# Kernel optimization log

Hardware: AMD Instinct MI355X
Metric: run time of the kernel (lower is better)

Reference implementation:

```python
import jax, jax.numpy as jnp
from jax import lax
import numpy as np

DIM = 8
C = 192
N = 198  # 2 special tokens + 14*14 patches (distilled=True)
B = 1024


def quick_gelu(x):
    return x * jax.nn.sigmoid(1.702 * x)


def setup_inputs() -> dict:
    key = jax.random.key(0)
    ks = jax.random.split(key, 7)
    return {
        "x": jax.random.normal(ks[0], (B, N, C), dtype=jnp.float32),
        "w_down": jax.random.normal(ks[1], (DIM, C), dtype=jnp.float32) * 0.05,
        "b_down": jnp.zeros((DIM,), dtype=jnp.float32),
        "conv_w": jax.random.normal(ks[2], (DIM, DIM, 3, 3), dtype=jnp.float32) * 0.05,
        "conv_b": jnp.zeros((DIM,), dtype=jnp.float32),
        "w_up": jax.random.normal(ks[3], (C, DIM), dtype=jnp.float32) * 0.05,
        "b_up": jnp.zeros((C,), dtype=jnp.float32),
    }


def _conv3x3(t, conv_w, conv_b):
    # t: [B, dim, H, W]; 3x3, stride 1, pad 1 (SAME)
    y = lax.conv_general_dilated(
        t, conv_w, window_strides=(1, 1), padding=((1, 1), (1, 1)),
        dimension_numbers=("NCHW", "OIHW", "NCHW"))
    return y + conv_b[None, :, None, None]


def reference(x, w_down, b_down, conv_w, conv_b, w_up, b_up):
    b, n, c = x.shape
    dim = w_down.shape[0]
    # down projection + QuickGELU
    d = quick_gelu(jnp.einsum("bnc,dc->bnd", x, w_down) + b_down)
    # patch tokens -> [B, dim, 14, 14] -> conv -> [B, 196, dim]
    x_patch = d[:, 2:].reshape(b, 14, 14, dim).transpose(0, 3, 1, 2)
    x_patch = _conv3x3(x_patch, conv_w, conv_b)
    x_patch = x_patch.transpose(0, 2, 3, 1).reshape(b, 14 * 14, dim)
    # cls token -> [B, dim, 1, 1] -> conv (only center tap contributes) -> [B, 1, dim]
    x_cls = d[:, :1].reshape(b, 1, 1, dim).transpose(0, 3, 1, 2)
    x_cls = _conv3x3(x_cls, conv_w, conv_b)
    x_cls = x_cls.transpose(0, 2, 3, 1).reshape(b, 1, dim)
    zero_dist = jnp.zeros_like(x_cls)
    d2 = jnp.concatenate([x_cls, zero_dist, x_patch], axis=1)
    d2 = quick_gelu(d2)  # dropout is identity in eval mode
    return jnp.einsum("bnd,cd->bnc", d2, w_up) + b_up
```

## Files before the change

### kernel.cpp

```cpp
#include <hip/hip_runtime.h>
#include <math.h>

#define NTOK 198
#define CCH  192

typedef float vf4 __attribute__((ext_vector_type(4)));

__device__ __forceinline__ float qgelu(float v) {
    return v / (1.0f + __expf(-1.702f * v));
}

__device__ __forceinline__ float dot8(const float4& a, const float4& wa,
                                      const float4& b, const float4& wb) {
    return a.x*wa.x + a.y*wa.y + a.z*wa.z + a.w*wa.w
         + b.x*wb.x + b.y*wb.y + b.z*wb.z + b.w*wb.w;
}

__global__ __launch_bounds__(512, 4) void convpass_fused(
    const float* __restrict__ x,
    const float* __restrict__ w_down,
    const float* __restrict__ b_down,
    const float* __restrict__ conv_w,
    const float* __restrict__ conv_b,
    const float* __restrict__ w_up,
    const float* __restrict__ b_up,
    float* __restrict__ out)
{
    const int b   = blockIdx.x;
    const int tid = threadIdx.x;

    __shared__ float s_d[NTOK * 8];
    __shared__ float s_d2[NTOK * 8];
    __shared__ float s_cw[576];
    __shared__ float s_cb[8];

    for (int t = tid; t < 576; t += 512) {
        const int kk = t >> 6, rem = t & 63, o = rem >> 3, i = rem & 7;
        s_cw[t] = conv_w[(o * 8 + i) * 9 + kk];
    }
    if (tid < 8) s_cb[tid] = conv_b[tid];

    {
        const int lane  = tid & 63;
        const int wv    = tid >> 6;
        const int chunk = lane >> 3;
        const int dim   = lane & 7;

        float wreg[24];
        {
            const float* wp = w_down + dim * CCH + chunk * 24;
            #pragma unroll
            for (int j = 0; j < 24; ++j) wreg[j] = wp[j];
        }
        const float bd  = b_down[dim];
        const float* xb = x + (size_t)b * NTOK * CCH + chunk * 24;

        const int nIter = (NTOK - wv + 7) >> 3;
        #pragma unroll 1
        for (int i = 0; i < nIter; ++i) {
            const int idx = i * 8 + wv;
            const bool valid = (idx < NTOK);
            const int n = valid ? idx : 0;
            const float* xr = xb + (size_t)n * CCH;
            float a0 = 0.f, a1 = 0.f;
            #pragma unroll
            for (int j = 0; j < 3; ++j) {
                const float4 xv = *(const float4*)(xr + j * 8);
                const float4 xw = *(const float4*)(xr + j * 8 + 4);
                a0 += xv.x*wreg[j*8]   + xv.y*wreg[j*8+1] + xv.z*wreg[j*8+2] + xv.w*wreg[j*8+3];
                a1 += xw.x*wreg[j*8+4] + xw.y*wreg[j*8+5] + xw.z*wreg[j*8+6] + xw.w*wreg[j*8+7];
            }
            float acc = a0 + a1;
            acc += __shfl_xor(acc, 8);
            acc += __shfl_xor(acc, 16);
            acc += __shfl_xor(acc, 32);
            if (valid && lane < 8) s_d[idx * 8 + dim] = qgelu(acc + bd);
        }
    }
    __syncthreads();

    for (int j = tid; j < NTOK * 4; j += 512) {
        const int n = j >> 2, o2 = j & 3;
        const int oA = o2, oB = o2 + 4;
        if (n == 1) {
            s_d2[n * 8 + oA] = 0.0f;
            s_d2[n * 8 + oB] = 0.0f;
        } else if (n == 0) {
            const float4 d0 = *(const float4*)&s_d[0];
            const float4 d1 = *(const float4*)&s_d[4];
            const float4 wa0 = *(const float4*)&s_cw[4 * 64 + oA * 8];
            const float4 wa1 = *(const float4*)&s_cw[4 * 64 + oA * 8 + 4];
            const float4 wb0 = *(const float4*)&s_cw[4 * 64 + oB * 8];
            const float4 wb1 = *(const float4*)&s_cw[4 * 64 + oB * 8 + 4];
            s_d2[n * 8 + oA] = qgelu(s_cb[oA] + dot8(d0, wa0, d1, wa1));
            s_d2[n * 8 + oB] = qgelu(s_cb[oB] + dot8(d0, wb0, d1, wb1));
        } else {
            const int pos = n - 2, h = pos / 14, w = pos % 14;
            float accA = s_cb[oA];
            float accB = s_cb[oB];
            #pragma unroll
            for (int dh = -1; dh <= 1; ++dh) {
                const int hh = h + dh;
                if (hh < 0 || hh > 13) continue;
                #pragma unroll
                for (int dw = -1; dw <= 1; ++dw) {
                    const int ww = w + dw;
                    if (ww < 0 || ww > 13) continue;
                    const int tok = 2 + hh * 14 + ww;
                    const int kk  = (dh + 1) * 3 + (dw + 1);
                    const float4 d0 = *(const float4*)&s_d[tok * 8];
                    const float4 d1 = *(const float4*)&s_d[tok * 8 + 4];
                    const float4 wa0 = *(const float4*)&s_cw[kk * 64 + oA * 8];
                    const float4 wa1 = *(const float4*)&s_cw[kk * 64 + oA * 8 + 4];
                    const float4 wb0 = *(const float4*)&s_cw[kk * 64 + oB * 8];
                    const float4 wb1 = *(const float4*)&s_cw[kk * 64 + oB * 8 + 4];
                    accA += dot8(d0, wa0, d1, wa1);
                    accB += dot8(d0, wb0, d1, wb1);
                }
            }
            s_d2[n * 8 + oA] = qgelu(accA);
            s_d2[n * 8 + oB] = qgelu(accB);
        }
    }
    __syncthreads();

    const int c4 = tid % 48;
    const int tl = tid / 48;
    if (tl < 10) {
        float w_r[4][8];
        #pragma unroll
        for (int cc = 0; cc < 4; ++cc) {
            const float4 wa = *(const float4*)(w_up + (c4 * 4 + cc) * 8);
            const float4 wb = *(const float4*)(w_up + (c4 * 4 + cc) * 8 + 4);
            w_r[cc][0] = wa.x; w_r[cc][1] = wa.y; w_r[cc][2] = wa.z; w_r[cc][3] = wa.w;
            w_r[cc][4] = wb.x; w_r[cc][5] = wb.y; w_r[cc][6] = wb.z; w_r[cc][7] = wb.w;
        }
        const float4 bu = *(const float4*)(b_up + c4 * 4);
        float* outb = out + (size_t)b * NTOK * CCH;
        #pragma unroll 1
        for (int nr = tl; nr < NTOK; nr += 10) {
            const float4 da = *(const float4*)&s_d2[nr * 8];
            const float4 dv = *(const float4*)&s_d2[nr * 8 + 4];
            float accs[4] = {bu.x, bu.y, bu.z, bu.w};
            #pragma unroll
            for (int cc = 0; cc < 4; ++cc) {
                accs[cc] += da.x * w_r[cc][0] + da.y * w_r[cc][1]
                          + da.z * w_r[cc][2] + da.w * w_r[cc][3]
                          + dv.x * w_r[cc][4] + dv.y * w_r[cc][5]
                          + dv.z * w_r[cc][6] + dv.w * w_r[cc][7];
            }
            const vf4 r = {accs[0], accs[1], accs[2], accs[3]};
            __builtin_nontemporal_store(r, (vf4*)(outb + (size_t)nr * CCH + c4 * 4));
        }
    }
}

extern "C" void kernel_launch(void* const* d_in, const int* in_sizes, int n_in,
                              void* d_out, int out_size, void* d_ws, size_t ws_size,
                              hipStream_t stream) {
    const float* x      = (const float*)d_in[0];
    const float* w_down = (const float*)d_in[1];
    const float* b_down = (const float*)d_in[2];
    const float* conv_w = (const float*)d_in[3];
    const float* conv_b = (const float*)d_in[4];
    const float* w_up   = (const float*)d_in[5];
    const float* b_up   = (const float*)d_in[6];
    float* out = (float*)d_out;

    const int B = in_sizes[0] / (NTOK * CCH);
    convpass_fused<<<dim3(B), dim3(512), 0, stream>>>(
        x, w_down, b_down, conv_w, conv_b, w_up, b_up, out);
}
```

Before: 75.73 us.

## Split each batch across two blocks along tokens with halo recomputation

Launches two blocks per batch element, each handling about half of the output tokens. Each block recomputes the down-projection for the extra rows of tokens the 3x3 conv needs at the split boundary, and shared-memory buffers shrink to match. The aim is more and smaller blocks, giving better load balance and more overlap between the down-projection, conv and up-projection phases across the GPU. The cost is redundant reads of about 26 rows of x per batch and extra down-projection compute.

Result: slower. 83.68 us (+10.5%).

```diff
diff --git a/kernel.cpp b/kernel.cpp
--- a/kernel.cpp
+++ b/kernel.cpp
@@ -26,11 +26,17 @@
     const float* __restrict__ b_up,
     float* __restrict__ out)
 {
-    const int b   = blockIdx.x;
-    const int tid = threadIdx.x;
+    const int half = blockIdx.x & 1;
+    const int b    = blockIdx.x >> 1;
+    const int tid  = threadIdx.x;
 
-    __shared__ float s_d[NTOK * 8];
-    __shared__ float s_d2[NTOK * 8];
+    const int d_start   = half ? 86  : 0;
+    const int d_count   = half ? 112 : 114;
+    const int out_start = half ? 100 : 0;
+    const int out_count = half ? 98  : 100;
+
+    __shared__ float s_d[114 * 8];
+    __shared__ float s_d2[100 * 8];
     __shared__ float s_cw[576];
     __shared__ float s_cb[8];
 
@@ -55,12 +61,12 @@
         const float bd  = b_down[dim];
         const float* xb = x + (size_t)b * NTOK * CCH + chunk * 24;
 
-        const int nIter = (NTOK - wv + 7) >> 3;
+        const int nIter = (d_count - wv + 7) >> 3;
         #pragma unroll 1
         for (int i = 0; i < nIter; ++i) {
             const int idx = i * 8 + wv;
-            const bool valid = (idx < NTOK);
-            const int n = valid ? idx : 0;
+            const bool valid = (idx < d_count);
+            const int n = d_start + (valid ? idx : 0);
             const float* xr = xb + (size_t)n * CCH;
             float a0 = 0.f, a1 = 0.f;
             #pragma unroll
@@ -79,12 +85,13 @@
     }
     __syncthreads();
 
-    for (int j = tid; j < NTOK * 4; j += 512) {
-        const int n = j >> 2, o2 = j & 3;
+    for (int j = tid; j < out_count * 4; j += 512) {
+        const int nr = j >> 2, o2 = j & 3;
         const int oA = o2, oB = o2 + 4;
+        const int n = out_start + nr;
         if (n == 1) {
-            s_d2[n * 8 + oA] = 0.0f;
-            s_d2[n * 8 + oB] = 0.0f;
+            s_d2[nr * 8 + oA] = 0.0f;
+            s_d2[nr * 8 + oB] = 0.0f;
         } else if (n == 0) {
             const float4 d0 = *(const float4*)&s_d[0];
             const float4 d1 = *(const float4*)&s_d[4];
@@ -92,8 +99,8 @@
             const float4 wa1 = *(const float4*)&s_cw[4 * 64 + oA * 8 + 4];
             const float4 wb0 = *(const float4*)&s_cw[4 * 64 + oB * 8];
             const float4 wb1 = *(const float4*)&s_cw[4 * 64 + oB * 8 + 4];
-            s_d2[n * 8 + oA] = qgelu(s_cb[oA] + dot8(d0, wa0, d1, wa1));
-            s_d2[n * 8 + oB] = qgelu(s_cb[oB] + dot8(d0, wb0, d1, wb1));
+            s_d2[nr * 8 + oA] = qgelu(s_cb[oA] + dot8(d0, wa0, d1, wa1));
+            s_d2[nr * 8 + oB] = qgelu(s_cb[oB] + dot8(d0, wb0, d1, wb1));
         } else {
             const int pos = n - 2, h = pos / 14, w = pos % 14;
             float accA = s_cb[oA];
@@ -108,8 +115,9 @@
                     if (ww < 0 || ww > 13) continue;
                     const int tok = 2 + hh * 14 + ww;
                     const int kk  = (dh + 1) * 3 + (dw + 1);
-                    const float4 d0 = *(const float4*)&s_d[tok * 8];
-                    const float4 d1 = *(const float4*)&s_d[tok * 8 + 4];
+                    const int ti  = tok - d_start;
+                    const float4 d0 = *(const float4*)&s_d[ti * 8];
+                    const float4 d1 = *(const float4*)&s_d[ti * 8 + 4];
                     const float4 wa0 = *(const float4*)&s_cw[kk * 64 + oA * 8];
                     const float4 wa1 = *(const float4*)&s_cw[kk * 64 + oA * 8 + 4];
                     const float4 wb0 = *(const float4*)&s_cw[kk * 64 + oB * 8];
@@ -118,8 +126,8 @@
                     accB += dot8(d0, wb0, d1, wb1);
                 }
             }
-            s_d2[n * 8 + oA] = qgelu(accA);
-            s_d2[n * 8 + oB] = qgelu(accB);
+            s_d2[nr * 8 + oA] = qgelu(accA);
+            s_d2[nr * 8 + oB] = qgelu(accB);
         }
     }
     __syncthreads();
@@ -136,9 +144,9 @@
             w_r[cc][4] = wb.x; w_r[cc][5] = wb.y; w_r[cc][6] = wb.z; w_r[cc][7] = wb.w;
         }
         const float4 bu = *(const float4*)(b_up + c4 * 4);
-        float* outb = out + (size_t)b * NTOK * CCH;
+        float* outb = out + ((size_t)b * NTOK + out_start) * CCH;
         #pragma unroll 1
-        for (int nr = tl; nr < NTOK; nr += 10) {
+        for (int nr = tl; nr < out_count; nr += 10) {
             const float4 da = *(const float4*)&s_d2[nr * 8];
             const float4 dv = *(const float4*)&s_d2[nr * 8 + 4];
             float accs[4] = {bu.x, bu.y, bu.z, bu.w};
@@ -168,6 +176,6 @@
     float* out = (float*)d_out;
 
     const int B = in_sizes[0] / (NTOK * CCH);
-    convpass_fused<<<dim3(B), dim3(512), 0, stream>>>(
+    convpass_fused<<<dim3(2 * B), dim3(512), 0, stream>>>(
         x, w_down, b_down, conv_w, conv_b, w_up, b_up, out);
 }
```

## Process two batch elements per 1024-thread block with warp-specialized overlap

Applied to the files above, without the earlier changes.

Each block now handles two batch elements with 1024 threads. Half the threads write the up-projection output of the first element while the other half run the down-projection for the second, so loads and stores overlap inside the block. This halves the grid and adds block-wide barriers. It also leaves phase C using only half the threads, and the second element's phase A runs on 8 waves instead of 16. The trade is less parallelism per phase for overlap of read and write traffic.

New measurement: 90.20 us. 19.1% more time.

```diff
diff --git a/kernel.cpp b/kernel.cpp
--- a/kernel.cpp
+++ b/kernel.cpp
@@ -16,70 +16,51 @@
          + b.x*wb.x + b.y*wb.y + b.z*wb.z + b.w*wb.w;
 }
 
-__global__ __launch_bounds__(512, 4) void convpass_fused(
-    const float* __restrict__ x,
-    const float* __restrict__ w_down,
-    const float* __restrict__ b_down,
-    const float* __restrict__ conv_w,
-    const float* __restrict__ conv_b,
-    const float* __restrict__ w_up,
-    const float* __restrict__ b_up,
-    float* __restrict__ out)
-{
-    const int b   = blockIdx.x;
-    const int tid = threadIdx.x;
-
-    __shared__ float s_d[NTOK * 8];
-    __shared__ float s_d2[NTOK * 8];
-    __shared__ float s_cw[576];
-    __shared__ float s_cb[8];
-
-    for (int t = tid; t < 576; t += 512) {
-        const int kk = t >> 6, rem = t & 63, o = rem >> 3, i = rem & 7;
-        s_cw[t] = conv_w[(o * 8 + i) * 9 + kk];
-    }
-    if (tid < 8) s_cb[tid] = conv_b[tid];
-
+template <int NW>
+__device__ __forceinline__ void phaseA(const float* __restrict__ x, int b,
+                                       const float* __restrict__ w_down,
+                                       const float* __restrict__ b_down,
+                                       float* s_d, int lane, int wv)
+{
+    const int chunk = lane >> 3;
+    const int dim   = lane & 7;
+    float wreg[24];
     {
-        const int lane  = tid & 63;
-        const int wv    = tid >> 6;
-        const int chunk = lane >> 3;
-        const int dim   = lane & 7;
-
-        float wreg[24];
-        {
-            const float* wp = w_down + dim * CCH + chunk * 24;
-            #pragma unroll
-            for (int j = 0; j < 24; ++j) wreg[j] = wp[j];
-        }
-        const float bd  = b_down[dim];
-        const float* xb = x + (size_t)b * NTOK * CCH + chunk * 24;
-
-        const int nIter = (NTOK - wv + 7) >> 3;
-        #pragma unroll 1
-        for (int i = 0; i < nIter; ++i) {
-            const int idx = i * 8 + wv;
-            const bool valid = (idx < NTOK);
-            const int n = valid ? idx : 0;
-            const float* xr = xb + (size_t)n * CCH;
-            float a0 = 0.f, a1 = 0.f;
-            #pragma unroll
-            for (int j = 0; j < 3; ++j) {
-                const float4 xv = *(const float4*)(xr + j * 8);
-                const float4 xw = *(const float4*)(xr + j * 8 + 4);
-                a0 += xv.x*wreg[j*8]   + xv.y*wreg[j*8+1] + xv.z*wreg[j*8+2] + xv.w*wreg[j*8+3];
-                a1 += xw.x*wreg[j*8+4] + xw.y*wreg[j*8+5] + xw.z*wreg[j*8+6] + xw.w*wreg[j*8+7];
-            }
-            float acc = a0 + a1;
-            acc += __shfl_xor(acc, 8);
-            acc += __shfl_xor(acc, 16);
-            acc += __shfl_xor(acc, 32);
-            if (valid && lane < 8) s_d[idx * 8 + dim] = qgelu(acc + bd);
-        }
-    }
-    __syncthreads();
-
-    for (int j = tid; j < NTOK * 4; j += 512) {
+        const float* wp = w_down + dim * CCH + chunk * 24;
+        #pragma unroll
+        for (int j = 0; j < 24; ++j) wreg[j] = wp[j];
+    }
+    const float bd  = b_down[dim];
+    const float* xb = x + (size_t)b * NTOK * CCH + chunk * 24;
+
+    const int nIter = (NTOK - wv + NW - 1) / NW;
+    #pragma unroll 1
+    for (int i = 0; i < nIter; ++i) {
+        const int idx = i * NW + wv;
+        const bool valid = (idx < NTOK);
+        const int n = valid ? idx : 0;
+        const float* xr = xb + (size_t)n * CCH;
+        float a0 = 0.f, a1 = 0.f;
+        #pragma unroll
+        for (int j = 0; j < 3; ++j) {
+            const float4 xv = *(const float4*)(xr + j * 8);
+            const float4 xw = *(const float4*)(xr + j * 8 + 4);
+            a0 += xv.x*wreg[j*8]   + xv.y*wreg[j*8+1] + xv.z*wreg[j*8+2] + xv.w*wreg[j*8+3];
+            a1 += xw.x*wreg[j*8+4] + xw.y*wreg[j*8+5] + xw.z*wreg[j*8+6] + xw.w*wreg[j*8+7];
+        }
+        float acc = a0 + a1;
+        acc += __shfl_xor(acc, 8);
+        acc += __shfl_xor(acc, 16);
+        acc += __shfl_xor(acc, 32);
+        if (valid && lane < 8) s_d[idx * 8 + dim] = qgelu(acc + bd);
+    }
+}
+
+template <int NTHR>
+__device__ __forceinline__ void phaseB(const float* s_d, float* s_d2,
+                                       const float* s_cw, const float* s_cb, int tid)
+{
+    for (int j = tid; j < NTOK * 4; j += NTHR) {
         const int n = j >> 2, o2 = j & 3;
         const int oA = o2, oB = o2 + 4;
         if (n == 1) {
@@ -122,10 +103,15 @@
             s_d2[n * 8 + oB] = qgelu(accB);
         }
     }
-    __syncthreads();
-
-    const int c4 = tid % 48;
-    const int tl = tid / 48;
+}
+
+__device__ __forceinline__ void phaseC(const float* s_d2,
+                                       const float* __restrict__ w_up,
+                                       const float* __restrict__ b_up,
+                                       float* __restrict__ out, int b, int t512)
+{
+    const int c4 = t512 % 48;
+    const int tl = t512 / 48;
     if (tl < 10) {
         float w_r[4][8];
         #pragma unroll
@@ -155,6 +141,51 @@
     }
 }
 
+__global__ __launch_bounds__(1024, 2) void convpass_fused(
+    const float* __restrict__ x,
+    const float* __restrict__ w_down,
+    const float* __restrict__ b_down,
+    const float* __restrict__ conv_w,
+    const float* __restrict__ conv_b,
+    const float* __restrict__ w_up,
+    const float* __restrict__ b_up,
+    float* __restrict__ out)
+{
+    const int e0  = blockIdx.x * 2;
+    const int e1  = e0 + 1;
+    const int tid = threadIdx.x;
+
+    __shared__ float s_d[NTOK * 8];
+    __shared__ float s_d2[NTOK * 8];
+    __shared__ float s_cw[576];
+    __shared__ float s_cb[8];
+
+    for (int t = tid; t < 576; t += 1024) {
+        const int kk = t >> 6, rem = t & 63, o = rem >> 3, i = rem & 7;
+        s_cw[t] = conv_w[(o * 8 + i) * 9 + kk];
+    }
+    if (tid < 8) s_cb[tid] = conv_b[tid];
+
+    const int lane = tid & 63;
+    const int wv16 = tid >> 6;
+
+    phaseA<16>(x, e0, w_down, b_down, s_d, lane, wv16);
+    __syncthreads();
+    phaseB<1024>(s_d, s_d2, s_cw, s_cb, tid);
+    __syncthreads();
+    if (tid < 512) {
+        phaseC(s_d2, w_up, b_up, out, e0, tid);
+    } else {
+        phaseA<8>(x, e1, w_down, b_down, s_d, lane, wv16 - 8);
+    }
+    __syncthreads();
+    phaseB<1024>(s_d, s_d2, s_cw, s_cb, tid);
+    __syncthreads();
+    if (tid < 512) {
+        phaseC(s_d2, w_up, b_up, out, e1, tid);
+    }
+}
+
 extern "C" void kernel_launch(void* const* d_in, const int* in_sizes, int n_in,
                               void* d_out, int out_size, void* d_ws, size_t ws_size,
                               hipStream_t stream) {
@@ -168,6 +199,6 @@
     float* out = (float*)d_out;
 
     const int B = in_sizes[0] / (NTOK * CCH);
-    convpass_fused<<<dim3(B), dim3(512), 0, stream>>>(
+    convpass_fused<<<dim3(B / 2), dim3(1024), 0, stream>>>(
         x, w_down, b_down, conv_w, conv_b, w_up, b_up, out);
 }
```
